# Kernel tuning notes

Hardware: AMD Instinct MI355X
Metric: run time of the kernel (lower is better)

Reference implementation:

```python
import jax, jax.numpy as jnp
import numpy as np

# Dims: B batch, T target seq, S source seq (self-attn: S==T), V symmetry-rep dim (D4 -> 8),
# M heads-per-group, K groups (num_heads = M*K = 8), F head_rep dim (TrivialRep -> 1),
# Hqk qk head width, Hv v head width, C feature width per rep component.
B, T, S, V, M, K, F, Hqk, Hv, C = 4, 512, 512, 8, 2, 4, 1, 32, 32, 256


def setup_inputs() -> dict:
    key = jax.random.key(0)
    ks = jax.random.split(key, 6)
    x = jax.random.normal(ks[0], (B, T, V, C), jnp.float32)
    # SymDecompLinear kernels: q has extra out reps (F, M, K); k/v have (F, 1, K) -> m axis broadcast
    Wq = jax.random.normal(ks[1], (C, M, K, F, Hqk), jnp.float32) / np.sqrt(C).astype(np.float32)
    Wk = jax.random.normal(ks[2], (C, K, F, Hqk), jnp.float32) / np.sqrt(C).astype(np.float32)
    Wv = jax.random.normal(ks[3], (C, K, F, Hv), jnp.float32) / np.sqrt(C).astype(np.float32)
    # out projection contracts the (M, K, F, Hv) head structure back to C features
    Wout = jax.random.normal(ks[4], (M, K, F, Hv, C), jnp.float32) / np.sqrt(M * K * F * Hv).astype(np.float32)
    mask = jax.random.bernoulli(ks[5], 0.9, (B, T, S))
    mask = mask.at[..., 0].set(True)  # guarantee each query attends to >=1 key
    return dict(x=x, Wq=Wq, Wk=Wk, Wv=Wv, Wout=Wout, mask=mask)


def reference(x, Wq, Wk, Wv, Wout, mask):
    # projections: q -> [B,T,V,M,K,F,Hqk]; k,v -> [B,S,V,K,F,H] (single head per group, broadcast over m)
    q = jnp.einsum('btvc,cmkfh->btvmkfh', x, Wq)
    k = jnp.einsum('bsvc,ckfh->bsvkfh', x, Wk)
    v = jnp.einsum('bsvc,ckfh->bsvkfh', x, Wv)
    scale = 1.0 / np.sqrt(F * Hqk).astype(np.float32)
    # logits retain the symmetry axis v: [B,T,S,V,M,K]
    logits = scale * jnp.einsum('btvmkfh,bsvkfh->btsvmk', q, k)
    lgmsk = mask[..., :, :, None, None, None]  # [B,T,S,1,1,1]
    weight = jax.nn.softmax(logits, axis=-4, where=lgmsk)  # softmax over source axis s
    att = jnp.einsum('btsvmk,bsvkfh->btvmkfh', weight, v)
    out = jnp.einsum('btvmkfh,mkfhc->btvc', att, Wout)
    return out
```

## Files before the change

kernel.cpp:

```cpp
#include <hip/hip_runtime.h>
#include <hip/hip_bf16.h>
#include <cstdint>

#define BB 4
#define TT 512
#define SS 512
#define VV 8
#define NROWS (BB * TT * VV)

typedef __attribute__((ext_vector_type(8))) short bf16x8;
typedef __attribute__((ext_vector_type(4))) float f32x4;

static __device__ __forceinline__ short f2bf(float f) {
  union { float f; unsigned u; } x; x.f = f;
  unsigned r = x.u + 0x7FFFu + ((x.u >> 16) & 1u);
  return (short)(r >> 16);
}

__global__ __launch_bounds__(256) void cvt_bf16_kernel(const float* __restrict__ in,
                                                       short* __restrict__ out) {
  int i = blockIdx.x * 256 + threadIdx.x;
  float4 a = ((const float4*)in)[2 * i];
  float4 b = ((const float4*)in)[2 * i + 1];
  bf16x8 o;
  o[0]=f2bf(a.x); o[1]=f2bf(a.y); o[2]=f2bf(a.z); o[3]=f2bf(a.w);
  o[4]=f2bf(b.x); o[5]=f2bf(b.y); o[6]=f2bf(b.z); o[7]=f2bf(b.w);
  ((bf16x8*)out)[i] = o;
}

__global__ __launch_bounds__(256) void pack_w_kernel(const float* __restrict__ Wq,
                                                     const float* __restrict__ Wk,
                                                     const float* __restrict__ Wv,
                                                     const float* __restrict__ Wout,
                                                     short* __restrict__ WcatT,
                                                     short* __restrict__ WoutT) {
  int idx = blockIdx.x * 256 + threadIdx.x;
  if (idx < 512 * 256) {
    int n = idx >> 8, c = idx & 255;
    float val;
    if (n < 256)      val = Wq[c * 256 + n] * 0.17677669529663687f;
    else if (n < 384) val = Wk[c * 128 + (n - 256)];
    else              val = Wv[c * 128 + (n - 384)];
    WcatT[idx] = f2bf(val);
  } else {
    int j = idx - 512 * 256;
    int cc = j >> 8, jj = j & 255;
    WoutT[j] = f2bf(Wout[jj * 256 + cc]);
  }
}

__global__ __launch_bounds__(256) void pack_mask_kernel(const int* __restrict__ mask,
                                                        unsigned long long* __restrict__ mask64) {
  int row = blockIdx.x * 4 + (threadIdx.x >> 6);
  int ln = threadIdx.x & 63;
  const int* mrow = mask + (size_t)row * SS;
#pragma unroll
  for (int c = 0; c < 8; ++c) {
    unsigned long long bal = __ballot(mrow[c * 64 + ln] != 0);
    if (ln == 0) mask64[(size_t)row * 8 + c] = bal;
  }
}

template <int N, bool OUTF32>
__global__ __launch_bounds__(256) void gemm_bf16(const short* __restrict__ A,
                                                 const short* __restrict__ Bt,
                                                 void* __restrict__ Cout) {
  __shared__ short As[128][64];
  __shared__ short Bs[128][64];
  const int tid = threadIdx.x;
  const int w = tid >> 6, ln = tid & 63;
  const int wr = (w >> 1) * 64, wc = (w & 1) * 64;
  const int bm = blockIdx.x * 128, bn = blockIdx.y * 128;
  const int lr = ln & 15, lk = (ln >> 4) * 8;
  const int r0 = tid >> 3, ko = (tid & 7) * 8;

  f32x4 acc[4][4] = {};

  for (int k0 = 0; k0 < 256; k0 += 64) {
    bf16x8 a0 = *(const bf16x8*)&A[(size_t)(bm + r0) * 256 + k0 + ko];
    bf16x8 a1 = *(const bf16x8*)&A[(size_t)(bm + 32 + r0) * 256 + k0 + ko];
    bf16x8 a2 = *(const bf16x8*)&A[(size_t)(bm + 64 + r0) * 256 + k0 + ko];
    bf16x8 a3 = *(const bf16x8*)&A[(size_t)(bm + 96 + r0) * 256 + k0 + ko];
    bf16x8 b0 = *(const bf16x8*)&Bt[(size_t)(bn + r0) * 256 + k0 + ko];
    bf16x8 b1 = *(const bf16x8*)&Bt[(size_t)(bn + 32 + r0) * 256 + k0 + ko];
    bf16x8 b2 = *(const bf16x8*)&Bt[(size_t)(bn + 64 + r0) * 256 + k0 + ko];
    bf16x8 b3 = *(const bf16x8*)&Bt[(size_t)(bn + 96 + r0) * 256 + k0 + ko];
    __syncthreads();
    *(bf16x8*)&As[r0][ko]      = a0;
    *(bf16x8*)&As[r0 + 32][ko] = a1;
    *(bf16x8*)&As[r0 + 64][ko] = a2;
    *(bf16x8*)&As[r0 + 96][ko] = a3;
    *(bf16x8*)&Bs[r0][ko]      = b0;
    *(bf16x8*)&Bs[r0 + 32][ko] = b1;
    *(bf16x8*)&Bs[r0 + 64][ko] = b2;
    *(bf16x8*)&Bs[r0 + 96][ko] = b3;
    __syncthreads();

#pragma unroll
    for (int kk = 0; kk < 2; ++kk) {
      bf16x8 af[4], bfr[4];
#pragma unroll
      for (int mi = 0; mi < 4; ++mi)
        af[mi] = *(const bf16x8*)&As[wr + mi * 16 + lr][kk * 32 + lk];
#pragma unroll
      for (int ni = 0; ni < 4; ++ni)
        bfr[ni] = *(const bf16x8*)&Bs[wc + ni * 16 + lr][kk * 32 + lk];
#pragma unroll
      for (int mi = 0; mi < 4; ++mi)
#pragma unroll
        for (int ni = 0; ni < 4; ++ni)
          acc[mi][ni] = __builtin_amdgcn_mfma_f32_16x16x32_bf16(af[mi], bfr[ni], acc[mi][ni], 0, 0, 0);
    }
  }

  const int rowg = (ln >> 4) * 4;
#pragma unroll
  for (int mi = 0; mi < 4; ++mi)
#pragma unroll
    for (int r = 0; r < 4; ++r) {
      size_t row = bm + wr + mi * 16 + rowg + r;
#pragma unroll
      for (int ni = 0; ni < 4; ++ni) {
        int col = bn + wc + ni * 16 + lr;
        if (OUTF32) ((float*)Cout)[row * N + col] = acc[mi][ni][r];
        else        ((short*)Cout)[row * N + col] = f2bf(acc[mi][ni][r]);
      }
    }
}

__global__ __launch_bounds__(256) void attn_mfma(const short* __restrict__ qkv,
                                                 const unsigned long long* __restrict__ mask64,
                                                 short* __restrict__ att) {
  const int t0 = blockIdx.x * 64;
  const int v  = blockIdx.y >> 2;
  const int k  = blockIdx.y & 3;
  const int b  = blockIdx.z;
  const int tid = threadIdx.x;
  const int w  = tid >> 6;
  const int ln = tid & 63;
  const int gq = ln >> 4;
  const int tr = ln & 15;

  __shared__ short Kt[2][64][40];
  __shared__ short Vt[2][32][72];
  __shared__ short Pt[4][16][72];

  bf16x8 qf[2];
  {
    const short* qp = qkv + ((size_t)((b*TT + t0 + w*16 + tr)*VV + v))*512 + k*32 + gq*8;
    qf[0] = *(const bf16x8*)qp;
    qf[1] = *(const bf16x8*)(qp + 128);
  }

  f32x4 acc_o[2][2] = {};
  float m_run[2] = {-1e30f, -1e30f};
  float l_run[2] = {0.f, 0.f};

  const int srow = tid >> 2;
  const int hg = (tid & 3) * 8;
  const unsigned long long* mrow = mask64 + ((size_t)(b*TT + t0 + w*16 + tr)) * 8;

  const short* src0 = qkv + ((size_t)((b*TT + srow)*VV + v))*512 + 256 + k*32 + hg;
  bf16x8 kreg = *(const bf16x8*)src0;
  bf16x8 vreg = *(const bf16x8*)(src0 + 128);

  for (int c = 0; c < 8; ++c) {
    const int cur = c & 1;
    *(bf16x8*)&Kt[cur][srow][hg] = kreg;
#pragma unroll
    for (int j = 0; j < 8; ++j) Vt[cur][hg + j][srow] = vreg[j];
    __syncthreads();
    if (c < 7) {
      const short* src = qkv + ((size_t)((b*TT + (c + 1) * 64 + srow)*VV + v))*512 + 256 + k*32 + hg;
      kreg = *(const bf16x8*)src;
      vreg = *(const bf16x8*)(src + 128);
    }
    unsigned long long mb = mrow[c];
    unsigned mlo = (unsigned)mb, mhi = (unsigned)(mb >> 32);
    float bias[4][4];
#pragma unroll
    for (int st = 0; st < 4; ++st) {
      unsigned wbits = (st < 2) ? mlo : mhi;
      const int base = (st & 1) * 16 + 4 * gq;
#pragma unroll
      for (int r = 0; r < 4; ++r)
        bias[st][r] = ((wbits >> (base + r)) & 1u) ? 0.f : -INFINITY;
    }

    bf16x8 kf[4], vf[2][2];
#pragma unroll
    for (int st = 0; st < 4; ++st) kf[st] = *(const bf16x8*)&Kt[cur][st*16 + tr][gq*8];
#pragma unroll
    for (int sh = 0; sh < 2; ++sh)
#pragma unroll
      for (int hh = 0; hh < 2; ++hh)
        vf[sh][hh] = *(const bf16x8*)&Vt[cur][hh*16 + tr][sh*32 + gq*8];

#pragma unroll
    for (int m = 0; m < 2; ++m) {
      f32x4 lac[4];
#pragma unroll
      for (int st = 0; st < 4; ++st) {
        f32x4 z = {0.f, 0.f, 0.f, 0.f};
        lac[st] = __builtin_amdgcn_mfma_f32_16x16x32_bf16(kf[st], qf[m], z, 0, 0, 0);
      }
      float pl[4][4];
#pragma unroll
      for (int st = 0; st < 4; ++st)
#pragma unroll
        for (int r = 0; r < 4; ++r)
          pl[st][r] = lac[st][r] + bias[st][r];

      float cm = -INFINITY;
#pragma unroll
      for (int st = 0; st < 4; ++st)
#pragma unroll
        for (int r = 0; r < 4; ++r) cm = fmaxf(cm, pl[st][r]);
      cm = fmaxf(cm, __shfl_xor(cm, 16));
      cm = fmaxf(cm, __shfl_xor(cm, 32));

      bool skip = __all(cm - m_run[m] <= 8.f);
      float mnew, corr;
      if (skip) { mnew = m_run[m]; corr = 1.f; }
      else {
        mnew = fmaxf(m_run[m], cm);
        corr = __expf(m_run[m] - mnew);
        m_run[m] = mnew;
      }

      float rs = 0.f;
#pragma unroll
      for (int st = 0; st < 4; ++st)
#pragma unroll
        for (int r = 0; r < 4; ++r) {
          pl[st][r] = __expf(pl[st][r] - mnew);
          rs += pl[st][r];
        }
      rs += __shfl_xor(rs, 16);
      rs += __shfl_xor(rs, 32);
      l_run[m] = l_run[m] * corr + rs;

      if (!skip) {
        float corrR[4];
#pragma unroll
        for (int r = 0; r < 4; ++r) corrR[r] = __shfl(corr, 4 * gq + r);
#pragma unroll
        for (int hh = 0; hh < 2; ++hh)
#pragma unroll
          for (int r = 0; r < 4; ++r) acc_o[m][hh][r] *= corrR[r];
      }

#pragma unroll
      for (int st = 0; st < 4; ++st) {
        unsigned d0 = ((unsigned)(unsigned short)f2bf(pl[st][1]) << 16) |
                      (unsigned)(unsigned short)f2bf(pl[st][0]);
        unsigned d1 = ((unsigned)(unsigned short)f2bf(pl[st][3]) << 16) |
                      (unsigned)(unsigned short)f2bf(pl[st][2]);
        *(uint2*)&Pt[w][tr][st * 16 + 4 * gq] = make_uint2(d0, d1);
      }
#pragma unroll
      for (int sh = 0; sh < 2; ++sh) {
        bf16x8 pf = *(const bf16x8*)&Pt[w][tr][sh * 32 + gq * 8];
#pragma unroll
        for (int hh = 0; hh < 2; ++hh)
          acc_o[m][hh] = __builtin_amdgcn_mfma_f32_16x16x32_bf16(pf, vf[sh][hh], acc_o[m][hh], 0, 0, 0);
      }
    }
  }

#pragma unroll
  for (int m = 0; m < 2; ++m) {
    float invR[4];
#pragma unroll
    for (int r = 0; r < 4; ++r) invR[r] = 1.f / __shfl(l_run[m], 4 * gq + r);
#pragma unroll
    for (int r = 0; r < 4; ++r) {
      short* dst = att + ((size_t)((b*TT + t0 + w*16 + 4*gq + r)*VV + v))*256
                 + m*128 + k*32 + tr;
      dst[0]  = f2bf(acc_o[m][0][r] * invR[r]);
      dst[16] = f2bf(acc_o[m][1][r] * invR[r]);
    }
  }
}

extern "C" void kernel_launch(void* const* d_in, const int* in_sizes, int n_in,
                              void* d_out, int out_size, void* d_ws, size_t ws_size,
                              hipStream_t stream) {
  const float* x = (const float*)d_in[0];
  const float* Wq = (const float*)d_in[1];
  const float* Wk = (const float*)d_in[2];
  const float* Wv = (const float*)d_in[3];
  const float* Wout = (const float*)d_in[4];
  const int* mask = (const int*)d_in[5];
  float* out = (float*)d_out;

  short* xb    = (short*)d_ws;
  short* WcatT = xb + (size_t)NROWS * 256;
  short* WoutT = WcatT + 512 * 256;
  short* qkv   = WoutT + 256 * 256;
  short* att   = qkv + (size_t)NROWS * 512;
  unsigned long long* mask64 = (unsigned long long*)(att + (size_t)NROWS * 256);

  cvt_bf16_kernel<<<NROWS * 256 / 8 / 256, 256, 0, stream>>>(x, xb);
  pack_w_kernel<<<(512 * 256 + 256 * 256) / 256, 256, 0, stream>>>(Wq, Wk, Wv, Wout, WcatT, WoutT);
  pack_mask_kernel<<<BB * TT / 4, 256, 0, stream>>>(mask, mask64);
  gemm_bf16<512, false><<<dim3(NROWS / 128, 4), 256, 0, stream>>>(xb, WcatT, qkv);
  attn_mfma<<<dim3(TT / 64, VV * 4, BB), 256, 0, stream>>>(qkv, mask64, att);
  gemm_bf16<256, true><<<dim3(NROWS / 128, 2), 256, 0, stream>>>(att, WoutT, out);
}
```

Before: 72.81 us.

## Fuse x bf16 conversion into QKV GEMM, widen attention blocks, use exp2 softmax

Drops the separate fp32-to-bf16 kernel for x and instead converts inside the QKV GEMM's global load, removing one launch and a round trip through a bf16 copy of x. The attention kernel now uses 512 threads covering 128 queries, with both halves of the block cooperatively loading two 64-key tiles per step, so each K/V tile is shared across more queries. Softmax switches to exp2 with log2(e) folded into the Wq scale, and the lazy-rescale threshold is raised to match the base-2 domain. In exchange the GEMM reads twice as many bytes for A, the attention grid has half as many blocks, and shared memory per block doubles.

```diff
diff --git a/kernel.cpp b/kernel.cpp
--- a/kernel.cpp
+++ b/kernel.cpp
@@ -15,17 +15,6 @@
   union { float f; unsigned u; } x; x.f = f;
   unsigned r = x.u + 0x7FFFu + ((x.u >> 16) & 1u);
   return (short)(r >> 16);
-}
-
-__global__ __launch_bounds__(256) void cvt_bf16_kernel(const float* __restrict__ in,
-                                                       short* __restrict__ out) {
-  int i = blockIdx.x * 256 + threadIdx.x;
-  float4 a = ((const float4*)in)[2 * i];
-  float4 b = ((const float4*)in)[2 * i + 1];
-  bf16x8 o;
-  o[0]=f2bf(a.x); o[1]=f2bf(a.y); o[2]=f2bf(a.z); o[3]=f2bf(a.w);
-  o[4]=f2bf(b.x); o[5]=f2bf(b.y); o[6]=f2bf(b.z); o[7]=f2bf(b.w);
-  ((bf16x8*)out)[i] = o;
 }
 
 __global__ __launch_bounds__(256) void pack_w_kernel(const float* __restrict__ Wq,
@@ -35,10 +24,11 @@
                                                      short* __restrict__ WcatT,
                                                      short* __restrict__ WoutT) {
   int idx = blockIdx.x * 256 + threadIdx.x;
+  const float qscale = 0.17677669529663687f * 1.4426950408889634f;
   if (idx < 512 * 256) {
     int n = idx >> 8, c = idx & 255;
     float val;
-    if (n < 256)      val = Wq[c * 256 + n] * 0.17677669529663687f;
+    if (n < 256)      val = Wq[c * 256 + n] * qscale;
     else if (n < 384) val = Wk[c * 128 + (n - 256)];
     else              val = Wv[c * 128 + (n - 384)];
     WcatT[idx] = f2bf(val);
@@ -61,8 +51,8 @@
   }
 }
 
-template <int N, bool OUTF32>
-__global__ __launch_bounds__(256) void gemm_bf16(const short* __restrict__ A,
+template <int N, bool AF32, bool OUTF32>
+__global__ __launch_bounds__(256) void gemm_bf16(const void* __restrict__ Ap,
                                                  const short* __restrict__ Bt,
                                                  void* __restrict__ Cout) {
   __shared__ short As[128][64];
@@ -77,23 +67,29 @@
   f32x4 acc[4][4] = {};
 
   for (int k0 = 0; k0 < 256; k0 += 64) {
-    bf16x8 a0 = *(const bf16x8*)&A[(size_t)(bm + r0) * 256 + k0 + ko];
-    bf16x8 a1 = *(const bf16x8*)&A[(size_t)(bm + 32 + r0) * 256 + k0 + ko];
-    bf16x8 a2 = *(const bf16x8*)&A[(size_t)(bm + 64 + r0) * 256 + k0 + ko];
-    bf16x8 a3 = *(const bf16x8*)&A[(size_t)(bm + 96 + r0) * 256 + k0 + ko];
-    bf16x8 b0 = *(const bf16x8*)&Bt[(size_t)(bn + r0) * 256 + k0 + ko];
-    bf16x8 b1 = *(const bf16x8*)&Bt[(size_t)(bn + 32 + r0) * 256 + k0 + ko];
-    bf16x8 b2 = *(const bf16x8*)&Bt[(size_t)(bn + 64 + r0) * 256 + k0 + ko];
-    bf16x8 b3 = *(const bf16x8*)&Bt[(size_t)(bn + 96 + r0) * 256 + k0 + ko];
+    bf16x8 a[4], bb[4];
+#pragma unroll
+    for (int i = 0; i < 4; ++i) {
+      size_t row = (size_t)(bm + i * 32 + r0);
+      if constexpr (AF32) {
+        const float* Af = (const float*)Ap;
+        float4 f0 = *(const float4*)&Af[row * 256 + k0 + ko];
+        float4 f1 = *(const float4*)&Af[row * 256 + k0 + ko + 4];
+        bf16x8 o;
+        o[0]=f2bf(f0.x); o[1]=f2bf(f0.y); o[2]=f2bf(f0.z); o[3]=f2bf(f0.w);
+        o[4]=f2bf(f1.x); o[5]=f2bf(f1.y); o[6]=f2bf(f1.z); o[7]=f2bf(f1.w);
+        a[i] = o;
+      } else {
+        a[i] = *(const bf16x8*)&((const short*)Ap)[row * 256 + k0 + ko];
+      }
+      bb[i] = *(const bf16x8*)&Bt[(size_t)(bn + i * 32 + r0) * 256 + k0 + ko];
+    }
     __syncthreads();
-    *(bf16x8*)&As[r0][ko]      = a0;
-    *(bf16x8*)&As[r0 + 32][ko] = a1;
-    *(bf16x8*)&As[r0 + 64][ko] = a2;
-    *(bf16x8*)&As[r0 + 96][ko] = a3;
-    *(bf16x8*)&Bs[r0][ko]      = b0;
-    *(bf16x8*)&Bs[r0 + 32][ko] = b1;
-    *(bf16x8*)&Bs[r0 + 64][ko] = b2;
-    *(bf16x8*)&Bs[r0 + 96][ko] = b3;
+#pragma unroll
+    for (int i = 0; i < 4; ++i) {
+      *(bf16x8*)&As[i * 32 + r0][ko] = a[i];
+      *(bf16x8*)&Bs[i * 32 + r0][ko] = bb[i];
+    }
     __syncthreads();
 
 #pragma unroll
@@ -128,10 +124,10 @@
     }
 }
 
-__global__ __launch_bounds__(256) void attn_mfma(const short* __restrict__ qkv,
+__global__ __launch_bounds__(512) void attn_mfma(const short* __restrict__ qkv,
                                                  const unsigned long long* __restrict__ mask64,
                                                  short* __restrict__ att) {
-  const int t0 = blockIdx.x * 64;
+  const int t0 = blockIdx.x * 128;
   const int v  = blockIdx.y >> 2;
   const int k  = blockIdx.y & 3;
   const int b  = blockIdx.z;
@@ -141,9 +137,9 @@
   const int gq = ln >> 4;
   const int tr = ln & 15;
 
-  __shared__ short Kt[2][64][40];
-  __shared__ short Vt[2][32][72];
-  __shared__ short Pt[4][16][72];
+  __shared__ short Kt[4][64][40];
+  __shared__ short Vt[4][32][72];
+  __shared__ short Pt[8][16][72];
 
   bf16x8 qf[2];
   {
@@ -156,114 +152,120 @@
   float m_run[2] = {-1e30f, -1e30f};
   float l_run[2] = {0.f, 0.f};
 
-  const int srow = tid >> 2;
-  const int hg = (tid & 3) * 8;
+  const int sp  = tid >> 8;
+  const int st2 = tid & 255;
+  const int srow = st2 >> 2;
+  const int hg = (st2 & 3) * 8;
   const unsigned long long* mrow = mask64 + ((size_t)(b*TT + t0 + w*16 + tr)) * 8;
 
-  const short* src0 = qkv + ((size_t)((b*TT + srow)*VV + v))*512 + 256 + k*32 + hg;
+  const short* src0 = qkv + ((size_t)((b*TT + sp*64 + srow)*VV + v))*512 + 256 + k*32 + hg;
   bf16x8 kreg = *(const bf16x8*)src0;
   bf16x8 vreg = *(const bf16x8*)(src0 + 128);
 
-  for (int c = 0; c < 8; ++c) {
-    const int cur = c & 1;
-    *(bf16x8*)&Kt[cur][srow][hg] = kreg;
-#pragma unroll
-    for (int j = 0; j < 8; ++j) Vt[cur][hg + j][srow] = vreg[j];
+  for (int c2 = 0; c2 < 4; ++c2) {
+    const int bufb = (c2 & 1) * 2;
+    *(bf16x8*)&Kt[bufb + sp][srow][hg] = kreg;
+#pragma unroll
+    for (int j = 0; j < 8; ++j) Vt[bufb + sp][hg + j][srow] = vreg[j];
     __syncthreads();
-    if (c < 7) {
-      const short* src = qkv + ((size_t)((b*TT + (c + 1) * 64 + srow)*VV + v))*512 + 256 + k*32 + hg;
+    if (c2 < 3) {
+      const short* src = qkv + ((size_t)((b*TT + (c2 + 1)*128 + sp*64 + srow)*VV + v))*512 + 256 + k*32 + hg;
       kreg = *(const bf16x8*)src;
       vreg = *(const bf16x8*)(src + 128);
     }
-    unsigned long long mb = mrow[c];
-    unsigned mlo = (unsigned)mb, mhi = (unsigned)(mb >> 32);
-    float bias[4][4];
-#pragma unroll
-    for (int st = 0; st < 4; ++st) {
-      unsigned wbits = (st < 2) ? mlo : mhi;
-      const int base = (st & 1) * 16 + 4 * gq;
-#pragma unroll
-      for (int r = 0; r < 4; ++r)
-        bias[st][r] = ((wbits >> (base + r)) & 1u) ? 0.f : -INFINITY;
-    }
-
-    bf16x8 kf[4], vf[2][2];
-#pragma unroll
-    for (int st = 0; st < 4; ++st) kf[st] = *(const bf16x8*)&Kt[cur][st*16 + tr][gq*8];
-#pragma unroll
-    for (int sh = 0; sh < 2; ++sh)
-#pragma unroll
-      for (int hh = 0; hh < 2; ++hh)
-        vf[sh][hh] = *(const bf16x8*)&Vt[cur][hh*16 + tr][sh*32 + gq*8];
-
-#pragma unroll
-    for (int m = 0; m < 2; ++m) {
-      f32x4 lac[4];
+
+#pragma unroll
+    for (int p = 0; p < 2; ++p) {
+      unsigned long long mb = mrow[2 * c2 + p];
+      unsigned mlo = (unsigned)mb, mhi = (unsigned)(mb >> 32);
+      float bias[4][4];
 #pragma unroll
       for (int st = 0; st < 4; ++st) {
-        f32x4 z = {0.f, 0.f, 0.f, 0.f};
-        lac[st] = __builtin_amdgcn_mfma_f32_16x16x32_bf16(kf[st], qf[m], z, 0, 0, 0);
+        unsigned wbits = (st < 2) ? mlo : mhi;
+        const int base = (st & 1) * 16 + 4 * gq;
+#pragma unroll
+        for (int r = 0; r < 4; ++r)
+          bias[st][r] = ((wbits >> (base + r)) & 1u) ? 0.f : -INFINITY;
       }
-      float pl[4][4];
-#pragma unroll
-      for (int st = 0; st < 4; ++st)
-#pragma unroll
-        for (int r = 0; r < 4; ++r)
-          pl[st][r] = lac[st][r] + bias[st][r];
-
-      float cm = -INFINITY;
-#pragma unroll
-      for (int st = 0; st < 4; ++st)
-#pragma unroll
-        for (int r = 0; r < 4; ++r) cm = fmaxf(cm, pl[st][r]);
-      cm = fmaxf(cm, __shfl_xor(cm, 16));
-      cm = fmaxf(cm, __shfl_xor(cm, 32));
-
-      bool skip = __all(cm - m_run[m] <= 8.f);
-      float mnew, corr;
-      if (skip) { mnew = m_run[m]; corr = 1.f; }
-      else {
-        mnew = fmaxf(m_run[m], cm);
-        corr = __expf(m_run[m] - mnew);
-        m_run[m] = mnew;
-      }
-
-      float rs = 0.f;
-#pragma unroll
-      for (int st = 0; st < 4; ++st)
-#pragma unroll
-        for (int r = 0; r < 4; ++r) {
-          pl[st][r] = __expf(pl[st][r] - mnew);
-          rs += pl[st][r];
-        }
-      rs += __shfl_xor(rs, 16);
-      rs += __shfl_xor(rs, 32);
-      l_run[m] = l_run[m] * corr + rs;
-
-      if (!skip) {
-        float corrR[4];
-#pragma unroll
-        for (int r = 0; r < 4; ++r) corrR[r] = __shfl(corr, 4 * gq + r);
+
+      bf16x8 kf[4], vf[2][2];
+#pragma unroll
+      for (int st = 0; st < 4; ++st) kf[st] = *(const bf16x8*)&Kt[bufb + p][st*16 + tr][gq*8];
+#pragma unroll
+      for (int sh = 0; sh < 2; ++sh)
 #pragma unroll
         for (int hh = 0; hh < 2; ++hh)
-#pragma unroll
-          for (int r = 0; r < 4; ++r) acc_o[m][hh][r] *= corrR[r];
-      }
-
-#pragma unroll
-      for (int st = 0; st < 4; ++st) {
-        unsigned d0 = ((unsigned)(unsigned short)f2bf(pl[st][1]) << 16) |
-                      (unsigned)(unsigned short)f2bf(pl[st][0]);
-        unsigned d1 = ((unsigned)(unsigned short)f2bf(pl[st][3]) << 16) |
-                      (unsigned)(unsigned short)f2bf(pl[st][2]);
-        *(uint2*)&Pt[w][tr][st * 16 + 4 * gq] = make_uint2(d0, d1);
-      }
-#pragma unroll
-      for (int sh = 0; sh < 2; ++sh) {
-        bf16x8 pf = *(const bf16x8*)&Pt[w][tr][sh * 32 + gq * 8];
-#pragma unroll
-        for (int hh = 0; hh < 2; ++hh)
-          acc_o[m][hh] = __builtin_amdgcn_mfma_f32_16x16x32_bf16(pf, vf[sh][hh], acc_o[m][hh], 0, 0, 0);
+          vf[sh][hh] = *(const bf16x8*)&Vt[bufb + p][hh*16 + tr][sh*32 + gq*8];
+
+#pragma unroll
+      for (int m = 0; m < 2; ++m) {
+        f32x4 lac[4];
+#pragma unroll
+        for (int st = 0; st < 4; ++st) {
+          f32x4 z = {0.f, 0.f, 0.f, 0.f};
+          lac[st] = __builtin_amdgcn_mfma_f32_16x16x32_bf16(kf[st], qf[m], z, 0, 0, 0);
+        }
+        float pl[4][4];
+#pragma unroll
+        for (int st = 0; st < 4; ++st)
+#pragma unroll
+          for (int r = 0; r < 4; ++r)
+            pl[st][r] = lac[st][r] + bias[st][r];
+
+        float cm = -INFINITY;
+#pragma unroll
+        for (int st = 0; st < 4; ++st)
+#pragma unroll
+          for (int r = 0; r < 4; ++r) cm = fmaxf(cm, pl[st][r]);
+        cm = fmaxf(cm, __shfl_xor(cm, 16));
+        cm = fmaxf(cm, __shfl_xor(cm, 32));
+
+        bool skip = __all(cm - m_run[m] <= 11.5f);
+        float mnew, corr;
+        if (skip) { mnew = m_run[m]; corr = 1.f; }
+        else {
+          mnew = fmaxf(m_run[m], cm);
+          corr = exp2f(m_run[m] - mnew);
+          m_run[m] = mnew;
+        }
+
+        float rs = 0.f;
+#pragma unroll
+        for (int st = 0; st < 4; ++st)
+#pragma unroll
+          for (int r = 0; r < 4; ++r) {
+            pl[st][r] = exp2f(pl[st][r] - mnew);
+            rs += pl[st][r];
+          }
+        rs += __shfl_xor(rs, 16);
+        rs += __shfl_xor(rs, 32);
+        l_run[m] = l_run[m] * corr + rs;
+
+        if (!skip) {
+          float corrR[4];
+#pragma unroll
+          for (int r = 0; r < 4; ++r) corrR[r] = __shfl(corr, 4 * gq + r);
+#pragma unroll
+          for (int hh = 0; hh < 2; ++hh)
+#pragma unroll
+            for (int r = 0; r < 4; ++r) acc_o[m][hh][r] *= corrR[r];
+        }
+
+#pragma unroll
+        for (int st = 0; st < 4; ++st) {
+          unsigned d0 = ((unsigned)(unsigned short)f2bf(pl[st][1]) << 16) |
+                        (unsigned)(unsigned short)f2bf(pl[st][0]);
+          unsigned d1 = ((unsigned)(unsigned short)f2bf(pl[st][3]) << 16) |
+                        (unsigned)(unsigned short)f2bf(pl[st][2]);
+          *(uint2*)&Pt[w][tr][st * 16 + 4 * gq] = make_uint2(d0, d1);
+        }
+#pragma unroll
+        for (int sh = 0; sh < 2; ++sh) {
+          bf16x8 pf = *(const bf16x8*)&Pt[w][tr][sh * 32 + gq * 8];
+#pragma unroll
+          for (int hh = 0; hh < 2; ++hh)
+            acc_o[m][hh] = __builtin_amdgcn_mfma_f32_16x16x32_bf16(pf, vf[sh][hh], acc_o[m][hh], 0, 0, 0);
+        }
       }
     }
   }
@@ -294,17 +296,15 @@
   const int* mask = (const int*)d_in[5];
   float* out = (float*)d_out;
 
-  short* xb    = (short*)d_ws;
-  short* WcatT = xb + (size_t)NROWS * 256;
+  short* WcatT = (short*)d_ws;
   short* WoutT = WcatT + 512 * 256;
   short* qkv   = WoutT + 256 * 256;
   short* att   = qkv + (size_t)NROWS * 512;
   unsigned long long* mask64 = (unsigned long long*)(att + (size_t)NROWS * 256);
 
-  cvt_bf16_kernel<<<NROWS * 256 / 8 / 256, 256, 0, stream>>>(x, xb);
   pack_w_kernel<<<(512 * 256 + 256 * 256) / 256, 256, 0, stream>>>(Wq, Wk, Wv, Wout, WcatT, WoutT);
   pack_mask_kernel<<<BB * TT / 4, 256, 0, stream>>>(mask, mask64);
-  gemm_bf16<512, false><<<dim3(NROWS / 128, 4), 256, 0, stream>>>(xb, WcatT, qkv);
-  attn_mfma<<<dim3(TT / 64, VV * 4, BB), 256, 0, stream>>>(qkv, mask64, att);
-  gemm_bf16<256, true><<<dim3(NROWS / 128, 2), 256, 0, stream>>>(att, WoutT, out);
-}
+  gemm_bf16<512, true, false><<<dim3(NROWS / 128, 4), 256, 0, stream>>>(x, WcatT, qkv);
+  attn_mfma<<<dim3(TT / 128, VV * 4, BB), 512, 0, stream>>>(qkv, mask64, att);
+  gemm_bf16<256, false, true><<<dim3(NROWS / 128, 2), 256, 0, stream>>>(att, WoutT, out);
+}
```

New measurement: 81.33 us. 11.7% more time.
